# Kernel optimization log

Hardware: AMD Instinct MI355X
Metric: run time of the kernel (lower is better)

Reference implementation:

```python
import jax, jax.numpy as jnp
import numpy as np

B, STATE_DIM, MLP_DIM, H, W = 128, 64, 512, 40, 40
LN_EPS = 1e-5


def _sobel_kernel(c):
    # Per-channel depthwise filters in torch order: [c0_sx, c0_sy, c0_id, c1_sx, ...]
    sx = jnp.array([[-1., 0., 1.], [-2., 0., 2.], [-1., 0., 1.]], jnp.float32)
    sy = jnp.array([[-1., -2., -1.], [0., 0., 0.], [1., 2., 1.]], jnp.float32)
    ident = jnp.array([[0., 0., 0.], [0., 1., 0.], [0., 0., 0.]], jnp.float32)
    k = jnp.stack([sx, sy, ident])[:, None]      # [3, 1, 3, 3]
    return jnp.tile(k, (c, 1, 1, 1))             # [3c, 1, 3, 3]


def setup_inputs() -> dict:
    key = jax.random.key(0)
    ks = jax.random.split(key, 6)
    state_in = jax.random.normal(ks[0], (B, STATE_DIM, H, W), jnp.float32)
    w1 = jax.random.normal(ks[1], (MLP_DIM, 3 * STATE_DIM), jnp.float32) * 0.05
    ln_weight = jax.random.uniform(ks[2], (MLP_DIM, H, W), jnp.float32, 0.5, 1.5)
    ln_bias = jax.random.normal(ks[3], (MLP_DIM, H, W), jnp.float32) * 0.01
    w2 = jax.random.normal(ks[4], (STATE_DIM, MLP_DIM), jnp.float32) * 0.05
    mask = jax.random.randint(ks[5], (H, W), 0, 2, jnp.int32)  # bernoulli(0.5) update mask
    return {"state_in": state_in, "w1": w1, "ln_weight": ln_weight,
            "ln_bias": ln_bias, "w2": w2, "mask": mask}


def reference(state_in, w1, ln_weight, ln_bias, w2, mask):
    C = state_in.shape[1]
    # Depthwise 3x3 sobel/identity perception: [B, C, H, W] -> [B, 3C, H, W]
    kern = _sobel_kernel(C)
    x = jax.lax.conv_general_dilated(
        state_in, kern, window_strides=(1, 1), padding='SAME',
        dimension_numbers=('NCHW', 'OIHW', 'NCHW'), feature_group_count=C)
    # 1x1 conv (no bias): [B, 3C, H, W] -> [B, MLP, H, W]
    x = jnp.einsum('bchw,oc->bohw', x, w1)
    # LayerNorm over (MLP, H, W) per sample, with elementwise affine
    mu = jnp.mean(x, axis=(1, 2, 3), keepdims=True)
    var = jnp.var(x, axis=(1, 2, 3), keepdims=True)
    x = (x - mu) * jax.lax.rsqrt(var + LN_EPS) * ln_weight + ln_bias
    x = jax.nn.relu(x)
    # 1x1 conv back to state channels (zero-init in original; random here for testing)
    x = jnp.einsum('bchw,oc->bohw', x, w2)
    # Stochastic per-pixel update mask, broadcast over batch and channels
    x = x * mask.astype(jnp.float32)
    # Alive mask: 3x3 max-pool on alive channel, stride 1, SAME padding
    live = jax.lax.reduce_window(state_in[:, 3], -jnp.inf, jax.lax.max,
                                 (1, 3, 3), (1, 1, 1), 'SAME')
    live = (live > 0.1).astype(jnp.float32)[:, None]  # [B, 1, H, W]
    return state_in + x * live
```

## Files before the change

kernel.cpp:

```cpp
#include <hip/hip_runtime.h>


typedef unsigned short u16;
typedef unsigned int   u32;
typedef __attribute__((ext_vector_type(8))) u16    ushort8;
typedef __attribute__((ext_vector_type(4))) u16    u16x4;
typedef __attribute__((ext_vector_type(8))) __bf16 bf16x8;
typedef __attribute__((ext_vector_type(4))) float  f32x4;
typedef __attribute__((ext_vector_type(4))) u32    u32x4;

#define NB   128
#define NC   64
#define K1   192
#define NO   512
#define NHW  1600
#define LN_N 819200.0f

__device__ __forceinline__ u16 f2bf(float f) {
    union { __bf16 h; u16 u; } v; v.h = (__bf16)f; return v.u;
}
__device__ __forceinline__ float bf2f(u16 h) {
    union { u32 u; float f; } v; v.u = ((u32)h) << 16; return v.f;
}
__device__ __forceinline__ float bfhi(u32 c) {
    union { u32 u; float f; } v; v.u = c & 0xffff0000u; return v.f;
}
__device__ __forceinline__ float bflo(u32 c) {
    union { u32 u; float f; } v; v.u = c << 16; return v.f;
}
__device__ __forceinline__ f32x4 mfma16(bf16x8 a, bf16x8 b, f32x4 c) {
    return __builtin_amdgcn_mfma_f32_16x16x32_bf16(a, b, c, 0, 0, 0);
}
__device__ __forceinline__ bf16x8 ldfrag(const u16* p) {
    return *(const bf16x8*)p;
}

__device__ __forceinline__ void load_halo(const float* __restrict__ base, int h,
                                          int wq, float reg[3][12]) {
#pragma unroll
    for (int jj = 0; jj < 3; ++jj) {
        int hh = h + jj - 1;
        bool vh = (unsigned)hh < 40u;
        const float* rowp = base + hh * 40;
#pragma unroll
        for (int i = 0; i < 12; ++i) {
            int col = wq * 10 - 1 + i;
            reg[jj][i] = (vh && (unsigned)col < 40u) ? rowp[col] : 0.0f;
        }
    }
}
__device__ __forceinline__ void sobel_px(const float reg[3][12], int t,
                                         float& sx, float& sy, float& idn) {
    sx = (reg[0][t + 2] - reg[0][t]) + 2.0f * (reg[1][t + 2] - reg[1][t])
       + (reg[2][t + 2] - reg[2][t]);
    sy = (reg[2][t] + 2.0f * reg[2][t + 1] + reg[2][t + 2])
       - (reg[0][t] + 2.0f * reg[0][t + 1] + reg[0][t + 2]);
    idn = reg[1][t + 1];
}

__global__ __launch_bounds__(256) void k0_all(const float* __restrict__ w1,
                                              const float* __restrict__ w2,
                                              const float* __restrict__ lnw,
                                              const float* __restrict__ lnb,
                                              u16* __restrict__ w1p,
                                              u16* __restrict__ w2p,
                                              u32* __restrict__ lnp,
                                              float* __restrict__ G,
                                              float* __restrict__ colw1,
                                              float* __restrict__ stats) {
    const int bid = blockIdx.x;
    const int tid = threadIdx.x;
    if (bid < 513) {
        int g = bid * 256 + tid;
        if (g < NO * K1) {
            u16 v = f2bf(w1[g]);
            int o = g / K1, k = g - o * K1;
            int f = o >> 4, ks = k >> 5;
            int lane = (((k >> 3) & 3) << 4) | (o & 15);
            w1p[(size_t)(((f * 6 + ks) * 64 + lane) * 8 + (k & 7))] = v;
        } else if (g < NO * K1 + NC * NO) {
            int i = g - NO * K1;
            int s = i / NO, o = i - s * NO;
            u16 v = f2bf(w2[i]);
            int wid = s >> 4, oc = o >> 6, ks2 = (o >> 5) & 1;
            int lane = (((o >> 3) & 3) << 4) | (s & 15);
            w2p[(size_t)((((wid * 8 + oc) * 2 + ks2) * 64 + lane) * 8 + (o & 7))] = v;
        } else if (g < NO * K1 + NC * NO + 256) {
            stats[g - NO * K1 - NC * NO] = 0.0f;
        }
    } else if (bid < 3713) {
        int g = (bid - 513) * 256 + tid;
        int o = g / NHW, p = g - o * NHW;
        int bx = p / 80, pr = p - bx * 80;
        int mi = pr >> 4, l15 = pr & 15;
        int oc = o >> 6, ro = o & 63;
        int wid = ro >> 4, hi = (ro >> 2) & 3, r = ro & 3;
        int lane = (hi << 4) | l15;
        int outi = ((((bx * 8 + oc) * 4 + wid) * 5 + mi) << 8) + lane * 4 + r;
        lnp[outi] = ((u32)f2bf(lnb[g]) << 16) | f2bf(lnw[g]);
    } else if (bid < 3749) {
        const int blk = bid - 3713;
        const int lane = tid & 63, wid = tid >> 6;
        const int q = lane >> 4, l15 = lane & 15;
        int bj = blk / 6, bk = blk - bj * 6;
        int j0 = bj * 32 + (wid & 1) * 16, k0 = bk * 32 + (wid >> 1) * 16;
        f32x4 acc = {0.f, 0.f, 0.f, 0.f};
        for (int ks = 0; ks < 16; ++ks) {
            union { u16 u[8]; bf16x8 v; } A, B;
#pragma unroll
            for (int j = 0; j < 8; ++j) {
                int o = ks * 32 + q * 8 + j;
                A.u[j] = f2bf(w1[(size_t)o * K1 + j0 + l15]);
                B.u[j] = f2bf(w1[(size_t)o * K1 + k0 + l15]);
            }
            acc = mfma16(A.v, B.v, acc);
        }
#pragma unroll
        for (int r = 0; r < 4; ++r)
            G[(size_t)(j0 + q * 4 + r) * K1 + k0 + l15] = acc[r];
    } else {
        if (tid < K1) {
            float s = 0.f;
#pragma unroll 8
            for (int o = 0; o < NO; ++o)
                s += bf2f(f2bf(w1[(size_t)o * K1 + tid]));
            colw1[tid] = s;
        }
    }
}

__global__ __launch_bounds__(256) void k2_stats(const float* __restrict__ state,
                                                const float* __restrict__ G,
                                                const float* __restrict__ colw1,
                                                float* __restrict__ stats) {
    const int bx = blockIdx.x;
    const int b  = blockIdx.y;
    const int h0 = bx * 2;
    const int tid = threadIdx.x;
    const int lane = tid & 63, wid = tid >> 6;
    const int q = lane >> 4, l15 = lane & 15;
    const int j0 = (wid & 1) * 96, j1 = (wid >> 1) * 96;

    __shared__ __align__(16) u16 Pt[192 * 104];
    __shared__ float red[8];

    for (int i = tid; i < 192 * 104 / 8; i += 256) ((u32x4*)Pt)[i] = (u32x4){0,0,0,0};
    __syncthreads();

    float psum0 = 0.f, psum1 = 0.f, psum2 = 0.f;
    const int c = tid >> 2, wq = tid & 3;
    {
        const float* base = state + ((size_t)b * NC + c) * NHW;
        for (int rr = 0; rr < 2; ++rr) {
            float reg[3][12];
            load_halo(base, h0 + rr, wq, reg);
#pragma unroll
            for (int t = 0; t < 10; ++t) {
                float sx, sy, idn; sobel_px(reg, t, sx, sy, idn);
                int px = rr * 40 + wq * 10 + t;
                u16 v0 = f2bf(sx), v1 = f2bf(sy), v2 = f2bf(idn);
                Pt[(3 * c + 0) * 104 + px] = v0;
                Pt[(3 * c + 1) * 104 + px] = v1;
                Pt[(3 * c + 2) * 104 + px] = v2;
                psum0 += bf2f(v0); psum1 += bf2f(v1); psum2 += bf2f(v2);
            }
        }
    }
    float sm = psum0 * colw1[3 * c] + psum1 * colw1[3 * c + 1]
             + psum2 * colw1[3 * c + 2];
    __syncthreads();

    float ssq = 0.f;
#pragma unroll 1
    for (int fi = 0; fi < 6; ++fi) {
        f32x4 acc[6];
#pragma unroll
        for (int j = 0; j < 6; ++j) { f32x4 z = {0.f,0.f,0.f,0.f}; acc[j] = z; }
#pragma unroll
        for (int ks = 0; ks < 3; ++ks) {
            bf16x8 av = ldfrag(&Pt[(j0 + fi * 16 + l15) * 104 + ks * 32 + q * 8]);
#pragma unroll
            for (int fj = 0; fj < 6; ++fj) {
                bf16x8 bv = ldfrag(&Pt[(j1 + fj * 16 + l15) * 104 + ks * 32 + q * 8]);
                acc[fj] = mfma16(av, bv, acc[fj]);
            }
        }
#pragma unroll
        for (int fj = 0; fj < 6; ++fj) {
            f32x4 gv = *(const f32x4*)&G[(size_t)(j1 + fj * 16 + l15) * K1
                                         + j0 + fi * 16 + q * 4];
#pragma unroll
            for (int r = 0; r < 4; ++r) ssq += acc[fj][r] * gv[r];
        }
    }

#pragma unroll
    for (int off = 32; off > 0; off >>= 1) {
        ssq += __shfl_down(ssq, off);
        sm  += __shfl_down(sm, off);
    }
    if (lane == 0) { red[wid] = ssq; red[4 + wid] = sm; }
    __syncthreads();
    if (tid == 0) {
        atomicAdd(&stats[b * 2],     red[4] + red[5] + red[6] + red[7]);
        atomicAdd(&stats[b * 2 + 1], red[0] + red[1] + red[2] + red[3]);
    }
}

__global__ __launch_bounds__(256, 3) void k4_fused(const float* __restrict__ state,
                                                   const u16* __restrict__ w1p,
                                                   const u16* __restrict__ w2p,
                                                   const u32* __restrict__ lnp,
                                                   const int* __restrict__ mask,
                                                   const float* __restrict__ stats,
                                                   float* __restrict__ out) {
    const int bx = blockIdx.x;
    const int b  = blockIdx.y;
    const int p0 = bx * 80, h0 = bx * 2;
    const int tid = threadIdx.x;
    const int lane = tid & 63, wid = tid >> 6;
    const int q = lane >> 4, l15 = lane & 15;

    __shared__ __align__(16) u16 Pt[80 * 192];
    __shared__ __align__(16) u16 Ys[80 * 64];

    const float s_sum = stats[2 * b], s_sq = stats[2 * b + 1];
    const float inv = 1.0f / LN_N;
    const float mu = s_sum * inv;
    const float var = s_sq * inv - mu * mu;
    const float rs = rsqrtf(var + 1e-5f);
    const float murs = mu * rs;

    {
        const int c = tid >> 2, wq = tid & 3;
        const float* base = state + ((size_t)b * NC + c) * NHW;
        for (int rr = 0; rr < 2; ++rr) {
            float reg[3][12];
            load_halo(base, h0 + rr, wq, reg);
#pragma unroll
            for (int t = 0; t < 10; ++t) {
                float sx, sy, idn; sobel_px(reg, t, sx, sy, idn);
                int px = rr * 40 + wq * 10 + t;
                int k = 3 * c;
#pragma unroll
                for (int i = 0; i < 3; ++i) {
                    int kk = k + i, u = kk >> 3;
                    int elem = px * 192 + (((u & 0x18) | ((u ^ px) & 7)) << 3) + (kk & 7);
                    Pt[elem] = f2bf(i == 0 ? sx : (i == 1 ? sy : idn));
                }
            }
        }
    }
    float g5[5];
    {
        const float* st3 = state + ((size_t)b * NC + 3) * NHW;
#pragma unroll
        for (int mi = 0; mi < 5; ++mi) {
            int p = p0 + mi * 16 + l15;
            int h = p / 40, w = p - h * 40;
            float mx = -1e30f;
#pragma unroll
            for (int dh = -1; dh <= 1; ++dh) {
                int hh = h + dh;
                if ((unsigned)hh < 40u)
#pragma unroll
                    for (int dw = -1; dw <= 1; ++dw) {
                        int wc = w + dw;
                        if ((unsigned)wc < 40u) mx = fmaxf(mx, st3[hh * 40 + wc]);
                    }
            }
            g5[mi] = (mx > 0.1f && mask[p] != 0) ? 1.0f : 0.0f;
        }
    }

    int pB0[5], pB1[5], yR0[5], yR1[5], yW[5];
    {
        const int q8 = q << 3;
        const int wu = wid * 2 + (q >> 1);
#pragma unroll
        for (int mi = 0; mi < 5; ++mi) {
            int r  = mi * 16 + l15;
            int xr = (r & 7) << 3;
            pB0[mi] = r * 192 + (q8 ^ xr);
            pB1[mi] = r * 192 + ((q8 + 32) ^ xr);
            int px = r & 7;
            yR0[mi] = r * 64 + ((q ^ px) << 3);
            yR1[mi] = r * 64 + (((q + 4) ^ px) << 3);
            yW[mi]  = r * 64 + ((wu ^ px) << 3) + (q & 1) * 4;
        }
    }

    bf16x8 a_cur[6];
    {
        const u16* w1base0 = w1p + ((size_t)(0 * 4 + wid) * 6) * 512 + lane * 8;
#pragma unroll
        for (int ks = 0; ks < 6; ++ks) a_cur[ks] = ldfrag(w1base0 + ks * 512);
    }
    __syncthreads();

    f32x4 acc2[5];
#pragma unroll
    for (int i = 0; i < 5; ++i) { f32x4 z = {0.f,0.f,0.f,0.f}; acc2[i] = z; }

    for (int oc = 0; oc < 8; ++oc) {
        u32x4 lv[5];
        {
            const u32* lb = lnp + ((((size_t)bx * 8 + oc) * 4 + wid) * 5) * 256 + lane * 4;
#pragma unroll
            for (int mi = 0; mi < 5; ++mi)
                lv[mi] = *(const u32x4*)(lb + mi * 256);
        }
        const u16* w2base = w2p + ((size_t)(wid * 8 + oc) * 2) * 512 + lane * 8;
        bf16x8 aw0 = ldfrag(w2base);
        bf16x8 aw1 = ldfrag(w2base + 512);

        const u16* w1next = w1p + ((size_t)((((oc + 1) & 7) * 4 + wid) * 6)) * 512
                          + lane * 8;
        f32x4 acc1[5];
#pragma unroll
        for (int i = 0; i < 5; ++i) { f32x4 z = {0.f,0.f,0.f,0.f}; acc1[i] = z; }
#pragma unroll
        for (int ks = 0; ks < 6; ++ks) {
            bf16x8 a = a_cur[ks];
            a_cur[ks] = ldfrag(w1next + ks * 512);
#pragma unroll
            for (int mi = 0; mi < 5; ++mi) {
                int off = ((ks & 1) ? pB1[mi] : pB0[mi]) + (ks >> 1) * 64;
                acc1[mi] = mfma16(a, ldfrag(&Pt[off]), acc1[mi]);
            }
        }
#pragma unroll
        for (int mi = 0; mi < 5; ++mi) {
            u16x4 yv;
#pragma unroll
            for (int r = 0; r < 4; ++r) {
                u32 cc = lv[mi][r];
                float t = fmaf(acc1[mi][r], rs, -murs);
                float y = fmaxf(fmaf(t, bflo(cc), bfhi(cc)), 0.0f);
                yv[r] = f2bf(y);
            }
            *(u16x4*)&Ys[yW[mi]] = yv;
        }
        __syncthreads();
#pragma unroll
        for (int ks2 = 0; ks2 < 2; ++ks2) {
            bf16x8 aw = ks2 ? aw1 : aw0;
#pragma unroll
            for (int mi = 0; mi < 5; ++mi) {
                int off = ks2 ? yR1[mi] : yR0[mi];
                acc2[mi] = mfma16(aw, ldfrag(&Ys[off]), acc2[mi]);
            }
        }
        __syncthreads();
    }

#pragma unroll
    for (int mi = 0; mi < 5; ++mi) {
        int p = p0 + mi * 16 + l15;
        float g = g5[mi];
#pragma unroll
        for (int r = 0; r < 4; ++r) {
            int s = wid * 16 + q * 4 + r;
            size_t idx = ((size_t)b * NC + s) * NHW + p;
            out[idx] = state[idx] + g * acc2[mi][r];
        }
    }
}

extern "C" void kernel_launch(void* const* d_in, const int* in_sizes, int n_in,
                              void* d_out, int out_size, void* d_ws, size_t ws_size,
                              hipStream_t stream) {
    const float* state = (const float*)d_in[0];
    const float* w1    = (const float*)d_in[1];
    const float* lnw   = (const float*)d_in[2];
    const float* lnb   = (const float*)d_in[3];
    const float* w2    = (const float*)d_in[4];
    const int*   mask  = (const int*)d_in[5];
    float* out = (float*)d_out;

    char* ws = (char*)d_ws;
    u16*    w1p   = (u16*)(ws + 0ull);
    u16*    w2p   = (u16*)(ws + 196608ull);
    u32*    lnp   = (u32*)(ws + 262144ull);
    float*  G     = (float*)(ws + 3735552ull);
    float*  colw1 = (float*)(ws + 3883008ull);
    float*  stats = (float*)(ws + 3883776ull);

    k0_all  <<<3750, 256, 0, stream>>>(w1, w2, lnw, lnb, w1p, w2p, lnp,
                                       G, colw1, stats);
    k2_stats<<<dim3(20, 128), 256, 0, stream>>>(state, G, colw1, stats);
    k4_fused<<<dim3(20, 128), 256, 0, stream>>>(state, w1p, w2p, lnp,
                                                mask, stats, out);
}
```

Before: 306.9 us.

## Double-buffer Ys in fused kernel and split Gram prep onto transposed bf16 w1

In the fused kernel, the shared Ys tile is now double-buffered by output chunk. This removes the trailing __syncthreads in each of the 8 iterations, so the next chunk's first GEMM can overlap the previous chunk's second GEMM. Separately, the prep kernel now also writes a transposed bf16 copy of w1. The Gram matrix and column sums move into a separate small kernel that uses vector loads from that copy instead of strided scalar fp32 loads and conversions. The cost is an extra launch and a dependency between the two prep kernels, plus 10 KB more LDS per block, which could threaten the 3-blocks-per-CU occupancy target.

```diff
diff --git a/kernel.cpp b/kernel.cpp
--- a/kernel.cpp
+++ b/kernel.cpp
@@ -58,16 +58,15 @@
     idn = reg[1][t + 1];
 }
 
-__global__ __launch_bounds__(256) void k0_all(const float* __restrict__ w1,
-                                              const float* __restrict__ w2,
-                                              const float* __restrict__ lnw,
-                                              const float* __restrict__ lnb,
-                                              u16* __restrict__ w1p,
-                                              u16* __restrict__ w2p,
-                                              u32* __restrict__ lnp,
-                                              float* __restrict__ G,
-                                              float* __restrict__ colw1,
-                                              float* __restrict__ stats) {
+__global__ __launch_bounds__(256) void k0_a(const float* __restrict__ w1,
+                                            const float* __restrict__ w2,
+                                            const float* __restrict__ lnw,
+                                            const float* __restrict__ lnb,
+                                            u16* __restrict__ w1p,
+                                            u16* __restrict__ w1T,
+                                            u16* __restrict__ w2p,
+                                            u32* __restrict__ lnp,
+                                            float* __restrict__ stats) {
     const int bid = blockIdx.x;
     const int tid = threadIdx.x;
     if (bid < 513) {
@@ -78,6 +77,7 @@
             int f = o >> 4, ks = k >> 5;
             int lane = (((k >> 3) & 3) << 4) | (o & 15);
             w1p[(size_t)(((f * 6 + ks) * 64 + lane) * 8 + (k & 7))] = v;
+            w1T[(size_t)k * NO + o] = v;
         } else if (g < NO * K1 + NC * NO) {
             int i = g - NO * K1;
             int s = i / NO, o = i - s * NO;
@@ -88,7 +88,7 @@
         } else if (g < NO * K1 + NC * NO + 256) {
             stats[g - NO * K1 - NC * NO] = 0.0f;
         }
-    } else if (bid < 3713) {
+    } else {
         int g = (bid - 513) * 256 + tid;
         int o = g / NHW, p = g - o * NHW;
         int bx = p / 80, pr = p - bx * 80;
@@ -98,34 +98,37 @@
         int lane = (hi << 4) | l15;
         int outi = ((((bx * 8 + oc) * 4 + wid) * 5 + mi) << 8) + lane * 4 + r;
         lnp[outi] = ((u32)f2bf(lnb[g]) << 16) | f2bf(lnw[g]);
-    } else if (bid < 3749) {
-        const int blk = bid - 3713;
-        const int lane = tid & 63, wid = tid >> 6;
-        const int q = lane >> 4, l15 = lane & 15;
+    }
+}
+
+__global__ __launch_bounds__(256) void k0_gram(const u16* __restrict__ w1T,
+                                               float* __restrict__ G,
+                                               float* __restrict__ colw1) {
+    const int blk = blockIdx.x;
+    const int tid = threadIdx.x;
+    const int lane = tid & 63, wid = tid >> 6;
+    const int q = lane >> 4, l15 = lane & 15;
+    if (blk < 36) {
         int bj = blk / 6, bk = blk - bj * 6;
         int j0 = bj * 32 + (wid & 1) * 16, k0 = bk * 32 + (wid >> 1) * 16;
         f32x4 acc = {0.f, 0.f, 0.f, 0.f};
+#pragma unroll
         for (int ks = 0; ks < 16; ++ks) {
-            union { u16 u[8]; bf16x8 v; } A, B;
-#pragma unroll
-            for (int j = 0; j < 8; ++j) {
-                int o = ks * 32 + q * 8 + j;
-                A.u[j] = f2bf(w1[(size_t)o * K1 + j0 + l15]);
-                B.u[j] = f2bf(w1[(size_t)o * K1 + k0 + l15]);
-            }
-            acc = mfma16(A.v, B.v, acc);
+            bf16x8 a  = ldfrag(&w1T[(size_t)(j0 + l15) * NO + ks * 32 + q * 8]);
+            bf16x8 bb = ldfrag(&w1T[(size_t)(k0 + l15) * NO + ks * 32 + q * 8]);
+            acc = mfma16(a, bb, acc);
         }
 #pragma unroll
         for (int r = 0; r < 4; ++r)
             G[(size_t)(j0 + q * 4 + r) * K1 + k0 + l15] = acc[r];
-    } else {
-        if (tid < K1) {
-            float s = 0.f;
-#pragma unroll 8
-            for (int o = 0; o < NO; ++o)
-                s += bf2f(f2bf(w1[(size_t)o * K1 + tid]));
-            colw1[tid] = s;
-        }
+    } else if (tid < K1) {
+        float s = 0.f;
+        for (int i = 0; i < NO / 8; ++i) {
+            ushort8 v = *(const ushort8*)&w1T[(size_t)tid * NO + i * 8];
+#pragma unroll
+            for (int j = 0; j < 8; ++j) s += bf2f(v[j]);
+        }
+        colw1[tid] = s;
     }
 }
 
@@ -222,7 +225,7 @@
     const int q = lane >> 4, l15 = lane & 15;
 
     __shared__ __align__(16) u16 Pt[80 * 192];
-    __shared__ __align__(16) u16 Ys[80 * 64];
+    __shared__ __align__(16) u16 Ys[2][80 * 64];
 
     const float s_sum = stats[2 * b], s_sq = stats[2 * b + 1];
     const float inv = 1.0f / LN_N;
@@ -303,6 +306,7 @@
     for (int i = 0; i < 5; ++i) { f32x4 z = {0.f,0.f,0.f,0.f}; acc2[i] = z; }
 
     for (int oc = 0; oc < 8; ++oc) {
+        u16* ys = Ys[oc & 1];
         u32x4 lv[5];
         {
             const u32* lb = lnp + ((((size_t)bx * 8 + oc) * 4 + wid) * 5) * 256 + lane * 4;
@@ -339,7 +343,7 @@
                 float y = fmaxf(fmaf(t, bflo(cc), bfhi(cc)), 0.0f);
                 yv[r] = f2bf(y);
             }
-            *(u16x4*)&Ys[yW[mi]] = yv;
+            *(u16x4*)&ys[yW[mi]] = yv;
         }
         __syncthreads();
 #pragma unroll
@@ -348,10 +352,9 @@
 #pragma unroll
             for (int mi = 0; mi < 5; ++mi) {
                 int off = ks2 ? yR1[mi] : yR0[mi];
-                acc2[mi] = mfma16(aw, ldfrag(&Ys[off]), acc2[mi]);
-            }
-        }
-        __syncthreads();
+                acc2[mi] = mfma16(aw, ldfrag(&ys[off]), acc2[mi]);
+            }
+        }
     }
 
 #pragma unroll
@@ -382,12 +385,13 @@
     u16*    w1p   = (u16*)(ws + 0ull);
     u16*    w2p   = (u16*)(ws + 196608ull);
     u32*    lnp   = (u32*)(ws + 262144ull);
+    u16*    w1T   = (u16*)(ws + 3538944ull);
     float*  G     = (float*)(ws + 3735552ull);
     float*  colw1 = (float*)(ws + 3883008ull);
     float*  stats = (float*)(ws + 3883776ull);
 
-    k0_all  <<<3750, 256, 0, stream>>>(w1, w2, lnw, lnb, w1p, w2p, lnp,
-                                       G, colw1, stats);
+    k0_a    <<<3713, 256, 0, stream>>>(w1, w2, lnw, lnb, w1p, w1T, w2p, lnp, stats);
+    k0_gram <<<37, 256, 0, stream>>>(w1T, G, colw1);
     k2_stats<<<dim3(20, 128), 256, 0, stream>>>(state, G, colw1, stats);
     k4_fused<<<dim3(20, 128), 256, 0, stream>>>(state, w1p, w2p, lnp,
                                                 mask, stats, out);
```

Result: faster. 296.8 us (-3.3%).
